# Kernel tuning notes

Hardware: AMD Instinct MI355X
Metric: run time of the kernel (lower is better)

## Reference

```python
import jax, jax.numpy as jnp
import numpy as np

N_NODES = 100000


def _mean_agg(x, src, dst, n_nodes):
    # mean of src-node features over in-edges of each dst node (DGL copy_u + mean)
    summed = jax.ops.segment_sum(x[src], dst, num_segments=n_nodes)  # [N, F]
    deg = jax.ops.segment_sum(jnp.ones_like(src, dtype=x.dtype), dst, num_segments=n_nodes)
    return summed / jnp.maximum(deg, 1.0)[:, None]  # nodes w/o in-edges -> 0


def _sage_conv(x, src, dst, W_self, W_neigh, b):
    # DGL SAGEConv('mean'): fc_self(h) + fc_neigh(mean_neigh(h)) + bias
    h_neigh = _mean_agg(x, src, dst, x.shape[0])
    return x @ W_self + h_neigh @ W_neigh + b


def setup_inputs() -> dict:
    key = jax.random.key(0)
    ks = jax.random.split(key, 8)
    F_IN, F_H, E = 128, 128, 1600000
    s = 1.0 / np.sqrt(F_IN)
    return {
        "x": jax.random.normal(ks[0], (N_NODES, F_IN), dtype=jnp.float32),
        "src": jax.random.randint(ks[1], (E,), 0, N_NODES, dtype=jnp.int64),
        "dst": jax.random.randint(ks[2], (E,), 0, N_NODES, dtype=jnp.int64),
        "W1_self": jax.random.normal(ks[3], (F_IN, F_H), dtype=jnp.float32) * s,
        "W1_neigh": jax.random.normal(ks[4], (F_IN, F_H), dtype=jnp.float32) * s,
        "b1": jnp.zeros((F_H,), dtype=jnp.float32),
        "W2_self": jax.random.normal(ks[5], (F_H, F_H), dtype=jnp.float32) * s,
        "W2_neigh": jax.random.normal(ks[6], (F_H, F_H), dtype=jnp.float32) * s,
        "b2": jnp.zeros((F_H,), dtype=jnp.float32),
    }


def reference(x, src, dst, W1_self, W1_neigh, b1, W2_self, W2_neigh, b2):
    h = _sage_conv(x, src, dst, W1_self, W1_neigh, b1)
    # dropout in eval mode == identity
    h = jax.nn.relu(h)
    return _sage_conv(h, src, dst, W2_self, W2_neigh, b2)
```

## Files before the change

### kernel.cpp

```cpp
#include <hip/hip_runtime.h>

#define F 128
#define NN 100000
#define NBUK 782
#define NBLK 256
#define LD 136
#define N4 (NN * F / 4)
#define N4A (N4 / 2)
#define SORT_CAP 8192

typedef __attribute__((ext_vector_type(8))) short short8;
typedef __attribute__((ext_vector_type(4))) float f32x4;
typedef __attribute__((ext_vector_type(4))) unsigned short us4;
typedef unsigned short ushort_t;

__device__ __forceinline__ ushort_t f2b(float f) {
    union { float f; unsigned u; } x;
    x.f = f;
    unsigned r = x.u + 0x7fffu + ((x.u >> 16) & 1u);
    return (ushort_t)(r >> 16);
}
__device__ __forceinline__ float b2f(ushort_t u) {
    union { unsigned u; float f; } x;
    x.u = ((unsigned)u) << 16;
    return x.f;
}

__global__ __launch_bounds__(256) void k1_fused(
    const int* __restrict__ dst, int* __restrict__ H, int E, int chunk,
    const float* __restrict__ Wa, const float* __restrict__ Wb,
    const float* __restrict__ Wc, const float* __restrict__ Wd,
    ushort_t* __restrict__ Oa, ushort_t* __restrict__ Ob,
    ushort_t* __restrict__ Oc, ushort_t* __restrict__ Od,
    const float* __restrict__ X, ushort_t* __restrict__ Y) {
    __shared__ union {
        int h[NBUK];
        float tile[32][33];
    } u;
    const int blk = blockIdx.x;
    if (blk < NBLK) {
        for (int i = threadIdx.x; i < NBUK; i += 256) u.h[i] = 0;
        __syncthreads();
        const int s0 = blk * chunk, s1 = min(E, s0 + chunk);
        for (int i = s0 + threadIdx.x; i < s1; i += 256)
            atomicAdd(&u.h[dst[i] >> 7], 1);
        __syncthreads();
        for (int i = threadIdx.x; i < NBUK; i += 256)
            H[blk * NBUK + i] = u.h[i];
    } else if (blk < NBLK + 64) {
        const int m = (blk - NBLK) >> 4;
        const int b = (blk - NBLK) & 15;
        const float* W = (m == 0) ? Wa : (m == 1) ? Wb : (m == 2) ? Wc : Wd;
        ushort_t* WT = (m == 0) ? Oa : (m == 1) ? Ob : (m == 2) ? Oc : Od;
        const int by = (b >> 2) * 32;
        const int bx = (b & 3) * 32;
        const int tx = threadIdx.x & 31, ty = threadIdx.x >> 5;
        for (int i = 0; i < 32; i += 8)
            u.tile[ty + i][tx] = W[(by + ty + i) * F + bx + tx];
        __syncthreads();
        for (int i = 0; i < 32; i += 8)
            WT[(bx + ty + i) * F + by + tx] = f2b(u.tile[tx][ty + i]);
    } else {
        const int i = (blk - NBLK - 64) * 256 + threadIdx.x;
        if (i < N4A) {
            float4 v = ((const float4*)X)[i];
            us4 o;
            o.x = f2b(v.x); o.y = f2b(v.y); o.z = f2b(v.z); o.w = f2b(v.w);
            ((us4*)Y)[i] = o;
        }
    }
}

__global__ __launch_bounds__(256) void scan_cols(int* __restrict__ H,
                                                 int* __restrict__ Htot) {
    __shared__ int s[NBLK];
    const int k = blockIdx.x;
    const int t = threadIdx.x;
    const int v = H[t * NBUK + k];
    s[t] = v;
    __syncthreads();
    for (int d = 1; d < NBLK; d <<= 1) {
        const int u = (t >= d) ? s[t - d] : 0;
        __syncthreads();
        s[t] += u;
        __syncthreads();
    }
    H[t * NBUK + k] = s[t] - v;
    if (t == NBLK - 1) Htot[k] = s[t];
}

__global__ __launch_bounds__(1024) void k2_fused(
    const int* __restrict__ Htot, int* __restrict__ boffs, int E,
    const float* __restrict__ X, ushort_t* __restrict__ Y) {
    if (blockIdx.x == 0) {
        __shared__ int tot[1024];
        const int k = threadIdx.x;
        const int v = (k < NBUK) ? Htot[k] : 0;
        tot[k] = v;
        __syncthreads();
        for (int d = 1; d < 1024; d <<= 1) {
            const int u = (k >= d) ? tot[k - d] : 0;
            __syncthreads();
            tot[k] += u;
            __syncthreads();
        }
        if (k < NBUK) boffs[k] = tot[k] - v;
        if (k == 0) boffs[NBUK] = E;
    } else {
        const int i = N4A + (blockIdx.x - 1) * 1024 + threadIdx.x;
        if (i < N4) {
            float4 v = ((const float4*)X)[i];
            us4 o;
            o.x = f2b(v.x); o.y = f2b(v.y); o.z = f2b(v.z); o.w = f2b(v.w);
            ((us4*)Y)[i] = o;
        }
    }
}

__global__ __launch_bounds__(256) void scatter2(const int* __restrict__ src,
                                                const int* __restrict__ dst,
                                                const int* __restrict__ H,
                                                const int* __restrict__ boffs,
                                                unsigned* __restrict__ pairs,
                                                int E, int chunk) {
    __shared__ int cur[NBUK];
    const int b = blockIdx.x;
    for (int i = threadIdx.x; i < NBUK; i += 256)
        cur[i] = boffs[i] + H[b * NBUK + i];
    __syncthreads();
    const int s0 = b * chunk, s1 = min(E, s0 + chunk);
    for (int i = s0 + threadIdx.x; i < s1; i += 256) {
        const int d = dst[i];
        const int p = atomicAdd(&cur[d >> 7], 1);
        pairs[p] = ((unsigned)(d & 127) << 20) | (unsigned)src[i];
    }
}

__global__ __launch_bounds__(256) void bucket_sort(const unsigned* __restrict__ pairs,
                                                   const int* __restrict__ boffs,
                                                   int* __restrict__ offs,
                                                   int* __restrict__ csr) {
    __shared__ int cnt[128], loffs[128], lcur[128];
    __shared__ int sbuf[SORT_CAP];
    const int b = blockIdx.x, t = threadIdx.x;
    const int e0 = boffs[b], e1 = boffs[b + 1];
    const int n = e1 - e0;
    const int node0 = b << 7;
    const int nnode = min(128, NN - node0);
    if (t < 128) cnt[t] = 0;
    __syncthreads();
    for (int i = e0 + t; i < e1; i += 256) atomicAdd(&cnt[pairs[i] >> 20], 1);
    __syncthreads();
    if (t < 128) loffs[t] = cnt[t];
    __syncthreads();
    for (int d = 1; d < 128; d <<= 1) {
        int u = (t >= d && t < 128) ? loffs[t - d] : 0;
        __syncthreads();
        if (t < 128) loffs[t] += u;
        __syncthreads();
    }
    if (t < 128) {
        const int ex = loffs[t] - cnt[t];
        if (t < nnode) offs[node0 + t] = e0 + ex;
    }
    if (b == NBUK - 1 && t == 0) offs[NN] = e1;

    if (n <= SORT_CAP) {
        if (t < 128) lcur[t] = loffs[t] - cnt[t];
        __syncthreads();
        for (int i = e0 + t; i < e1; i += 256) {
            const unsigned v = pairs[i];
            const int p = atomicAdd(&lcur[v >> 20], 1);
            sbuf[p] = (int)(v & 0xFFFFFu);
        }
        __syncthreads();
        if (t < 128) {
            const int lo = loffs[t] - cnt[t];
            const int hi = loffs[t];
            for (int i = lo + 1; i < hi; ++i) {
                const int key = sbuf[i];
                int j = i - 1;
                while (j >= lo && sbuf[j] > key) { sbuf[j + 1] = sbuf[j]; --j; }
                sbuf[j + 1] = key;
            }
        }
        __syncthreads();
        for (int i = t; i < n; i += 256) csr[e0 + i] = sbuf[i];
    } else {
        if (t < 128) lcur[t] = e0 + (loffs[t] - cnt[t]);
        __syncthreads();
        for (int i = e0 + t; i < e1; i += 256) {
            const unsigned v = pairs[i];
            const int p = atomicAdd(&lcur[v >> 20], 1);
            csr[p] = (int)(v & 0xFFFFFu);
        }
    }
}

template <typename TOUT>
__global__ __launch_bounds__(256, 8) void sage_layer(
    const ushort_t* __restrict__ Xg,
    const int* __restrict__ offs, const int* __restrict__ csr,
    const ushort_t* __restrict__ WTs, const ushort_t* __restrict__ WTn,
    const float* __restrict__ bias,
    TOUT* __restrict__ out, int relu) {
    __shared__ __align__(16) ushort_t sX[32 * LD];
    __shared__ __align__(16) ushort_t sH[32 * LD];
    const int t = threadIdx.x;
    const int lane = t & 63;
    const int wave = t >> 6;
    const int brow0 = blockIdx.x * 32;

    {
        const ushort_t* base = Xg + (size_t)brow0 * F;
        for (int i = t; i < 32 * 16; i += 256) {
            int row = i >> 4, ch = i & 15;
            *(short8*)&sX[row * LD + ch * 8] = *(const short8*)&base[row * F + ch * 8];
        }
    }

    {
        const int slot = lane >> 4;
        const int cl = lane & 15;
        const int c8 = cl * 8;
#pragma unroll
        for (int rr = 0; rr < 2; rr++) {
            const int rloc = wave * 8 + slot * 2 + rr;
            const int row = brow0 + rloc;
            const int e0 = offs[row], e1 = offs[row + 1];
            float a0[8], a1[8], a2[8], a3[8];
#pragma unroll
            for (int j = 0; j < 8; j++) { a0[j] = a1[j] = a2[j] = a3[j] = 0.f; }
            int e = e0;
            for (; e + 3 < e1; e += 4) {
                const int s0 = csr[e], s1 = csr[e + 1], s2 = csr[e + 2], s3 = csr[e + 3];
                const short8 v0 = *(const short8*)&Xg[(size_t)s0 * F + c8];
                const short8 v1 = *(const short8*)&Xg[(size_t)s1 * F + c8];
                const short8 v2 = *(const short8*)&Xg[(size_t)s2 * F + c8];
                const short8 v3 = *(const short8*)&Xg[(size_t)s3 * F + c8];
#pragma unroll
                for (int j = 0; j < 8; j++) {
                    a0[j] += b2f((ushort_t)v0[j]);
                    a1[j] += b2f((ushort_t)v1[j]);
                    a2[j] += b2f((ushort_t)v2[j]);
                    a3[j] += b2f((ushort_t)v3[j]);
                }
            }
            for (; e < e1; e++) {
                const int s0 = csr[e];
                const short8 v0 = *(const short8*)&Xg[(size_t)s0 * F + c8];
#pragma unroll
                for (int j = 0; j < 8; j++) a0[j] += b2f((ushort_t)v0[j]);
            }
            const float inv = (e1 > e0) ? (1.0f / (float)(e1 - e0)) : 0.f;
            short8 o;
#pragma unroll
            for (int j = 0; j < 8; j++)
                o[j] = (short)f2b(((a0[j] + a1[j]) + (a2[j] + a3[j])) * inv);
            *(short8*)&sH[rloc * LD + c8] = o;
        }
    }
    __syncthreads();

    const int q = lane >> 4, nl = lane & 15;
    const int colbase = wave * 32;
    f32x4 acc00 = (f32x4)0.f, acc01 = (f32x4)0.f, acc10 = (f32x4)0.f, acc11 = (f32x4)0.f;
#pragma unroll
    for (int ks = 0; ks < 4; ks++) {
        const int ko = ks * 32 + q * 8;
        const short8 aS0 = *(const short8*)&sX[nl * LD + ko];
        const short8 aS1 = *(const short8*)&sX[(16 + nl) * LD + ko];
        const short8 aN0 = *(const short8*)&sH[nl * LD + ko];
        const short8 aN1 = *(const short8*)&sH[(16 + nl) * LD + ko];
        const size_t bo0 = (size_t)(colbase + nl) * F + ko;
        const size_t bo1 = (size_t)(colbase + 16 + nl) * F + ko;
        const short8 bS0 = *(const short8*)&WTs[bo0];
        const short8 bS1 = *(const short8*)&WTs[bo1];
        const short8 bN0 = *(const short8*)&WTn[bo0];
        const short8 bN1 = *(const short8*)&WTn[bo1];
        acc00 = __builtin_amdgcn_mfma_f32_16x16x32_bf16(aS0, bS0, acc00, 0, 0, 0);
        acc00 = __builtin_amdgcn_mfma_f32_16x16x32_bf16(aN0, bN0, acc00, 0, 0, 0);
        acc01 = __builtin_amdgcn_mfma_f32_16x16x32_bf16(aS0, bS1, acc01, 0, 0, 0);
        acc01 = __builtin_amdgcn_mfma_f32_16x16x32_bf16(aN0, bN1, acc01, 0, 0, 0);
        acc10 = __builtin_amdgcn_mfma_f32_16x16x32_bf16(aS1, bS0, acc10, 0, 0, 0);
        acc10 = __builtin_amdgcn_mfma_f32_16x16x32_bf16(aN1, bN0, acc10, 0, 0, 0);
        acc11 = __builtin_amdgcn_mfma_f32_16x16x32_bf16(aS1, bS1, acc11, 0, 0, 0);
        acc11 = __builtin_amdgcn_mfma_f32_16x16x32_bf16(aN1, bN1, acc11, 0, 0, 0);
    }

    const float b0 = bias[colbase + nl];
    const float b1 = bias[colbase + 16 + nl];
    if constexpr (sizeof(TOUT) == 2) {
        __syncthreads();
#pragma unroll
        for (int r = 0; r < 4; r++) {
            const int lr0 = q * 4 + r, lr1 = 16 + q * 4 + r;
            float v00 = acc00[r] + b0, v01 = acc01[r] + b1;
            float v10 = acc10[r] + b0, v11 = acc11[r] + b1;
            if (relu) {
                v00 = fmaxf(v00, 0.f); v01 = fmaxf(v01, 0.f);
                v10 = fmaxf(v10, 0.f); v11 = fmaxf(v11, 0.f);
            }
            sX[lr0 * LD + colbase + nl] = f2b(v00);
            sX[lr0 * LD + colbase + 16 + nl] = f2b(v01);
            sX[lr1 * LD + colbase + nl] = f2b(v10);
            sX[lr1 * LD + colbase + 16 + nl] = f2b(v11);
        }
        __syncthreads();
        TOUT* base = out + (size_t)brow0 * F;
        for (int i = t; i < 32 * 16; i += 256) {
            int row = i >> 4, ch = i & 15;
            *(short8*)&base[row * F + ch * 8] = *(const short8*)&sX[row * LD + ch * 8];
        }
    } else {
#pragma unroll
        for (int r = 0; r < 4; r++) {
            const int orow0 = brow0 + q * 4 + r;
            const int orow1 = brow0 + 16 + q * 4 + r;
            float v00 = acc00[r] + b0, v01 = acc01[r] + b1;
            float v10 = acc10[r] + b0, v11 = acc11[r] + b1;
            if (relu) {
                v00 = fmaxf(v00, 0.f); v01 = fmaxf(v01, 0.f);
                v10 = fmaxf(v10, 0.f); v11 = fmaxf(v11, 0.f);
            }
            out[(size_t)orow0 * F + colbase + nl] = v00;
            out[(size_t)orow0 * F + colbase + 16 + nl] = v01;
            out[(size_t)orow1 * F + colbase + nl] = v10;
            out[(size_t)orow1 * F + colbase + 16 + nl] = v11;
        }
    }
}

extern "C" void kernel_launch(void* const* d_in, const int* in_sizes, int n_in,
                              void* d_out, int out_size, void* d_ws, size_t ws_size,
                              hipStream_t stream) {
    const float* x = (const float*)d_in[0];
    const int* src = (const int*)d_in[1];
    const int* dst = (const int*)d_in[2];
    const float* W1s = (const float*)d_in[3];
    const float* W1n = (const float*)d_in[4];
    const float* b1 = (const float*)d_in[5];
    const float* W2s = (const float*)d_in[6];
    const float* W2n = (const float*)d_in[7];
    const float* b2 = (const float*)d_in[8];
    float* out = (float*)d_out;

    const int E = in_sizes[1];
    const int N = NN;
    const int E4 = (E + 3) & ~3;
    const int chunk = (E + NBLK - 1) / NBLK;

    unsigned* pairs = (unsigned*)d_ws;
    int* csr = (int*)(pairs + E4);
    ushort_t* h1 = (ushort_t*)(csr + E4);
    ushort_t* WT1s = h1 + (size_t)N * F;
    ushort_t* WT1n = WT1s + F * F;
    ushort_t* WT2s = WT1n + F * F;
    ushort_t* WT2n = WT2s + F * F;
    int* offs = (int*)(WT2n + F * F);
    int* H = offs + (N + 1);
    int* boffs = H + NBLK * NBUK;
    int* Htot = boffs + (NBUK + 1);
    ushort_t* xb = (ushort_t*)d_out;

    const int cvtA_blocks = (N4A + 255) / 256;
    k1_fused<<<NBLK + 64 + cvtA_blocks, 256, 0, stream>>>(
        dst, H, E, chunk, W1s, W1n, W2s, W2n, WT1s, WT1n, WT2s, WT2n, x, xb);
    scan_cols<<<NBUK, NBLK, 0, stream>>>(H, Htot);
    const int cvtB_blocks = (N4 - N4A + 1023) / 1024;
    k2_fused<<<1 + cvtB_blocks, 1024, 0, stream>>>(Htot, boffs, E, x, xb);
    scatter2<<<NBLK, 256, 0, stream>>>(src, dst, H, boffs, pairs, E, chunk);
    bucket_sort<<<NBUK, 256, 0, stream>>>(pairs, boffs, offs, csr);

    sage_layer<ushort_t><<<N / 32, 256, 0, stream>>>(
        xb, offs, csr, WT1s, WT1n, b1, h1, 1);
    sage_layer<float><<<N / 32, 256, 0, stream>>>(
        h1, offs, csr, WT2s, WT2n, b2, out, 0);
}
```

Measured before the change: 382.9 us.

## Replace per-node insertion sort with parallel rank sort; unroll gather by 8

The bucket sort kernel drops the serial per-node insertion sort, run by only 128 threads, in favour of a rank-based placement. Every thread counts how many entries in its node's segment are smaller and writes its element straight to that rank in csr, so all 256 threads take part and the extra sort pass is removed. The aggregation loop now issues 8 independent neighbour row loads per iteration into a single accumulator, raising memory-level parallelism in the gather. The fallback path also changes its csr index to e0+p because lcur now holds bucket-local offsets.

```diff
diff --git a/kernel.cpp b/kernel.cpp
--- a/kernel.cpp
+++ b/kernel.cpp
@@ -141,7 +141,7 @@
                                                    int* __restrict__ offs,
                                                    int* __restrict__ csr) {
     __shared__ int cnt[128], loffs[128], lcur[128];
-    __shared__ int sbuf[SORT_CAP];
+    __shared__ unsigned sbuf[SORT_CAP];
     const int b = blockIdx.x, t = threadIdx.x;
     const int e0 = boffs[b], e1 = boffs[b + 1];
     const int n = e1 - e0;
@@ -161,38 +161,36 @@
     }
     if (t < 128) {
         const int ex = loffs[t] - cnt[t];
+        lcur[t] = ex;
         if (t < nnode) offs[node0 + t] = e0 + ex;
     }
     if (b == NBUK - 1 && t == 0) offs[NN] = e1;
+    __syncthreads();
 
     if (n <= SORT_CAP) {
-        if (t < 128) lcur[t] = loffs[t] - cnt[t];
-        __syncthreads();
         for (int i = e0 + t; i < e1; i += 256) {
             const unsigned v = pairs[i];
             const int p = atomicAdd(&lcur[v >> 20], 1);
-            sbuf[p] = (int)(v & 0xFFFFFu);
-        }
-        __syncthreads();
-        if (t < 128) {
-            const int lo = loffs[t] - cnt[t];
-            const int hi = loffs[t];
-            for (int i = lo + 1; i < hi; ++i) {
-                const int key = sbuf[i];
-                int j = i - 1;
-                while (j >= lo && sbuf[j] > key) { sbuf[j + 1] = sbuf[j]; --j; }
-                sbuf[j + 1] = key;
-            }
-        }
-        __syncthreads();
-        for (int i = t; i < n; i += 256) csr[e0 + i] = sbuf[i];
+            sbuf[p] = v;
+        }
+        __syncthreads();
+        for (int i = t; i < n; i += 256) {
+            const unsigned v = sbuf[i];
+            const int d = v >> 20;
+            const int hi = loffs[d];
+            const int lo = hi - cnt[d];
+            int r = lo;
+            for (int j = lo; j < hi; ++j) {
+                const unsigned w = sbuf[j];
+                r += (w < v) || (w == v && j < i);
+            }
+            csr[e0 + r] = (int)(v & 0xFFFFFu);
+        }
     } else {
-        if (t < 128) lcur[t] = e0 + (loffs[t] - cnt[t]);
-        __syncthreads();
         for (int i = e0 + t; i < e1; i += 256) {
             const unsigned v = pairs[i];
             const int p = atomicAdd(&lcur[v >> 20], 1);
-            csr[p] = (int)(v & 0xFFFFFu);
+            csr[e0 + p] = (int)(v & 0xFFFFFu);
         }
     }
 }
@@ -228,10 +226,30 @@
             const int rloc = wave * 8 + slot * 2 + rr;
             const int row = brow0 + rloc;
             const int e0 = offs[row], e1 = offs[row + 1];
-            float a0[8], a1[8], a2[8], a3[8];
-#pragma unroll
-            for (int j = 0; j < 8; j++) { a0[j] = a1[j] = a2[j] = a3[j] = 0.f; }
+            float acc[8];
+#pragma unroll
+            for (int j = 0; j < 8; j++) acc[j] = 0.f;
             int e = e0;
+            for (; e + 7 < e1; e += 8) {
+                const int s0 = csr[e],     s1 = csr[e + 1], s2 = csr[e + 2], s3 = csr[e + 3];
+                const int s4 = csr[e + 4], s5 = csr[e + 5], s6 = csr[e + 6], s7 = csr[e + 7];
+                const short8 v0 = *(const short8*)&Xg[(size_t)s0 * F + c8];
+                const short8 v1 = *(const short8*)&Xg[(size_t)s1 * F + c8];
+                const short8 v2 = *(const short8*)&Xg[(size_t)s2 * F + c8];
+                const short8 v3 = *(const short8*)&Xg[(size_t)s3 * F + c8];
+                const short8 v4 = *(const short8*)&Xg[(size_t)s4 * F + c8];
+                const short8 v5 = *(const short8*)&Xg[(size_t)s5 * F + c8];
+                const short8 v6 = *(const short8*)&Xg[(size_t)s6 * F + c8];
+                const short8 v7 = *(const short8*)&Xg[(size_t)s7 * F + c8];
+#pragma unroll
+                for (int j = 0; j < 8; j++) {
+                    const float t01 = b2f((ushort_t)v0[j]) + b2f((ushort_t)v1[j]);
+                    const float t23 = b2f((ushort_t)v2[j]) + b2f((ushort_t)v3[j]);
+                    const float t45 = b2f((ushort_t)v4[j]) + b2f((ushort_t)v5[j]);
+                    const float t67 = b2f((ushort_t)v6[j]) + b2f((ushort_t)v7[j]);
+                    acc[j] += (t01 + t23) + (t45 + t67);
+                }
+            }
             for (; e + 3 < e1; e += 4) {
                 const int s0 = csr[e], s1 = csr[e + 1], s2 = csr[e + 2], s3 = csr[e + 3];
                 const short8 v0 = *(const short8*)&Xg[(size_t)s0 * F + c8];
@@ -240,23 +258,21 @@
                 const short8 v3 = *(const short8*)&Xg[(size_t)s3 * F + c8];
 #pragma unroll
                 for (int j = 0; j < 8; j++) {
-                    a0[j] += b2f((ushort_t)v0[j]);
-                    a1[j] += b2f((ushort_t)v1[j]);
-                    a2[j] += b2f((ushort_t)v2[j]);
-                    a3[j] += b2f((ushort_t)v3[j]);
+                    const float t01 = b2f((ushort_t)v0[j]) + b2f((ushort_t)v1[j]);
+                    const float t23 = b2f((ushort_t)v2[j]) + b2f((ushort_t)v3[j]);
+                    acc[j] += t01 + t23;
                 }
             }
             for (; e < e1; e++) {
                 const int s0 = csr[e];
                 const short8 v0 = *(const short8*)&Xg[(size_t)s0 * F + c8];
 #pragma unroll
-                for (int j = 0; j < 8; j++) a0[j] += b2f((ushort_t)v0[j]);
+                for (int j = 0; j < 8; j++) acc[j] += b2f((ushort_t)v0[j]);
             }
             const float inv = (e1 > e0) ? (1.0f / (float)(e1 - e0)) : 0.f;
             short8 o;
 #pragma unroll
-            for (int j = 0; j < 8; j++)
-                o[j] = (short)f2b(((a0[j] + a1[j]) + (a2[j] + a3[j])) * inv);
+            for (int j = 0; j < 8; j++) o[j] = (short)f2b(acc[j] * inv);
             *(short8*)&sH[rloc * LD + c8] = o;
         }
     }
```

After: 340.8 us. 11.0% less time.
